# Kernel optimization log

Hardware: AMD Instinct MI355X
Metric: run time of the kernel (lower is better)

## Reference

```python
import jax, jax.numpy as jnp
import numpy as np

TP = 4
TOKENS = 8192
HIDDEN = 4096
EPS = 1e-6
FP8_MAX = 448.0  # float8_e4m3fn max


def setup_inputs() -> dict:
    key = jax.random.key(0)
    k1, k2, k3 = jax.random.split(key, 3)
    hidden_states = jax.random.normal(k1, (TP, TOKENS, HIDDEN), dtype=jnp.float32)
    residual = jax.random.normal(k2, (TOKENS, HIDDEN), dtype=jnp.float32)
    weight = jax.random.uniform(k3, (HIDDEN,), dtype=jnp.float32)
    return {"hidden_states": hidden_states, "residual": residual, "weight": weight}


def rms_norm(x, weight, eps):
    # vLLM RMSNorm: x * rsqrt(mean(x^2) + eps) * weight, computed in fp32
    var = jnp.mean(jnp.square(x), axis=-1, keepdims=True)
    return x * jax.lax.rsqrt(var + eps) * weight


def scaled_fp8_quant(x):
    # dynamic per-tensor fp8 quantization: scale = amax / FP8_MAX
    amax = jnp.max(jnp.abs(x))
    scale = jnp.maximum(amax, 1e-12) / FP8_MAX
    q = jnp.clip(x / scale, -FP8_MAX, FP8_MAX)  # quantized values (kept fp32 for reference math)
    return q, scale


def reference(hidden_states, residual, weight):
    # tensor_model_parallel_all_reduce == sum over TP shards (leading axis)
    all_reduce = jnp.sum(hidden_states, axis=0)  # [TOKENS, HIDDEN]
    normed = rms_norm(all_reduce, weight, EPS)
    q, scale = scaled_fp8_quant(normed)
    return q, scale
```

## Files before the change

kernel.cpp:

```cpp
#include <hip/hip_runtime.h>
#include <hip/hip_fp16.h>

#define TOKENS_ 8192
#define HIDDEN_ 4096
#define EPS_ 1e-6f
#define FP8MAX_ 448.0f

typedef float f32x4 __attribute__((ext_vector_type(4)));
typedef unsigned int u32x4 __attribute__((ext_vector_type(4)));

static constexpr size_t NELEM = (size_t)TOKENS_ * HIDDEN_;
static constexpr size_t WS_SCALE_OFF = 0;
static constexpr size_t WS_BMAX_OFF = 4096;
static constexpr size_t WS_H16_OFF = 65536;
static constexpr size_t WS_NEEDED = WS_H16_OFF + NELEM * sizeof(unsigned short);

static __device__ inline unsigned int pack_half2(float a, float b) {
    __half2 h = __floats2half2_rn(a, b);
    return *reinterpret_cast<unsigned int*>(&h);
}
static __device__ inline float2 unpack_half2(unsigned int u) {
    return __half22float2(*reinterpret_cast<const __half2*>(&u));
}
static __device__ inline float clip1(float x, float invs) {
    return fminf(fmaxf(x * invs, -FP8MAX_), FP8MAX_);
}

__global__ __launch_bounds__(256) void k_norm_h(
    const float* __restrict__ hs, const float* __restrict__ w,
    unsigned int* __restrict__ normed_h2, float* __restrict__ bmax_arr)
{
    const int row = blockIdx.x;
    const int tid = threadIdx.x;
    const size_t S4 = NELEM / 4;
    const f32x4* __restrict__ base =
        reinterpret_cast<const f32x4*>(hs) + (size_t)row * (HIDDEN_ / 4);
    const f32x4* __restrict__ w4 = reinterpret_cast<const f32x4*>(w);

    f32x4 sv[4];
    float ss = 0.f;
#pragma unroll
    for (int j = 0; j < 4; ++j) {
        const size_t idx = (size_t)tid + j * 256;
        f32x4 a = __builtin_nontemporal_load(&base[idx]);
        f32x4 b = __builtin_nontemporal_load(&base[idx + S4]);
        f32x4 c = __builtin_nontemporal_load(&base[idx + 2 * S4]);
        f32x4 d = __builtin_nontemporal_load(&base[idx + 3 * S4]);
        f32x4 s = (a + b) + (c + d);
        sv[j] = s;
        ss += s.x * s.x + s.y * s.y + s.z * s.z + s.w * s.w;
    }

    __shared__ float red[4];
#pragma unroll
    for (int off = 32; off > 0; off >>= 1) ss += __shfl_down(ss, off, 64);
    const int wave = tid >> 6;
    if ((tid & 63) == 0) red[wave] = ss;
    __syncthreads();
    ss = red[0] + red[1] + red[2] + red[3];
    const float inv = rsqrtf(ss * (1.0f / HIDDEN_) + EPS_);

    uint2* __restrict__ out =
        reinterpret_cast<uint2*>(normed_h2) + (size_t)row * (HIDDEN_ / 4);
    float am = 0.f;
#pragma unroll
    for (int j = 0; j < 4; ++j) {
        const size_t idx = (size_t)tid + j * 256;
        f32x4 wv = w4[idx];
        f32x4 o = sv[j] * inv * wv;
        uint2 p;
        p.x = pack_half2(o.x, o.y);
        p.y = pack_half2(o.z, o.w);
        out[idx] = p;
        am = fmaxf(am, fmaxf(fmaxf(fabsf(o.x), fabsf(o.y)),
                             fmaxf(fabsf(o.z), fabsf(o.w))));
    }

    __shared__ float redm[4];
#pragma unroll
    for (int off = 32; off > 0; off >>= 1)
        am = fmaxf(am, __shfl_down(am, off, 64));
    if ((tid & 63) == 0) redm[wave] = am;
    __syncthreads();
    if (tid == 0)
        bmax_arr[row] = fmaxf(fmaxf(redm[0], redm[1]), fmaxf(redm[2], redm[3]));
}

__global__ __launch_bounds__(256) void k_quant_h2(
    const unsigned int* __restrict__ normed_h2,
    const float* __restrict__ bmax_arr, float* __restrict__ q_out,
    float* __restrict__ scale_out)
{
    const int tid = threadIdx.x;
    const f32x4* __restrict__ b4 = reinterpret_cast<const f32x4*>(bmax_arr);
    float am = 0.f;
#pragma unroll
    for (int j = 0; j < 8; ++j) {
        f32x4 v = b4[tid + j * 256];
        am = fmaxf(am, fmaxf(fmaxf(v.x, v.y), fmaxf(v.z, v.w)));
    }
    __shared__ float red[4];
#pragma unroll
    for (int off = 32; off > 0; off >>= 1)
        am = fmaxf(am, __shfl_down(am, off, 64));
    if ((tid & 63) == 0) red[tid >> 6] = am;
    __syncthreads();
    am = fmaxf(fmaxf(red[0], red[1]), fmaxf(red[2], red[3]));
    const float scale = fmaxf(am, 1e-12f) / FP8MAX_;
    const float invs = 1.0f / scale;
    if (blockIdx.x == 0 && tid == 0) scale_out[0] = scale;

    const size_t n8 = NELEM / 8;
    const u32x4* __restrict__ src = reinterpret_cast<const u32x4*>(normed_h2);
    f32x4* __restrict__ dst = reinterpret_cast<f32x4*>(q_out);
    const size_t stride = (size_t)gridDim.x * blockDim.x;
    for (size_t i = (size_t)blockIdx.x * blockDim.x + tid; i < n8;
         i += stride) {
        u32x4 u = src[i];
        float2 f0 = unpack_half2(u.x);
        float2 f1 = unpack_half2(u.y);
        float2 f2 = unpack_half2(u.z);
        float2 f3 = unpack_half2(u.w);
        f32x4 a, b;
        a.x = clip1(f0.x, invs);
        a.y = clip1(f0.y, invs);
        a.z = clip1(f1.x, invs);
        a.w = clip1(f1.y, invs);
        b.x = clip1(f2.x, invs);
        b.y = clip1(f2.y, invs);
        b.z = clip1(f3.x, invs);
        b.w = clip1(f3.y, invs);
        __builtin_nontemporal_store(a, &dst[i * 2]);
        __builtin_nontemporal_store(b, &dst[i * 2 + 1]);
    }
}


__global__ __launch_bounds__(256) void k_fused_norm_f(
    const float* __restrict__ hs, const float* __restrict__ w,
    float* __restrict__ normed, float* __restrict__ bmax_arr)
{
    const int row = blockIdx.x;
    const int tid = threadIdx.x;
    const size_t S4 = NELEM / 4;
    const f32x4* __restrict__ base =
        reinterpret_cast<const f32x4*>(hs) + (size_t)row * (HIDDEN_ / 4);
    const f32x4* __restrict__ w4 = reinterpret_cast<const f32x4*>(w);
    f32x4 sv[4];
    float ss = 0.f;
#pragma unroll
    for (int j = 0; j < 4; ++j) {
        const size_t idx = (size_t)tid + j * 256;
        f32x4 a = base[idx];
        f32x4 b = base[idx + S4];
        f32x4 c = base[idx + 2 * S4];
        f32x4 d = base[idx + 3 * S4];
        f32x4 s = (a + b) + (c + d);
        sv[j] = s;
        ss += s.x * s.x + s.y * s.y + s.z * s.z + s.w * s.w;
    }
    __shared__ float red[4];
#pragma unroll
    for (int off = 32; off > 0; off >>= 1) ss += __shfl_down(ss, off, 64);
    const int wave = tid >> 6;
    if ((tid & 63) == 0) red[wave] = ss;
    __syncthreads();
    ss = red[0] + red[1] + red[2] + red[3];
    const float inv = rsqrtf(ss * (1.0f / HIDDEN_) + EPS_);
    f32x4* __restrict__ out =
        reinterpret_cast<f32x4*>(normed) + (size_t)row * (HIDDEN_ / 4);
    float am = 0.f;
#pragma unroll
    for (int j = 0; j < 4; ++j) {
        const size_t idx = (size_t)tid + j * 256;
        f32x4 wv = w4[idx];
        f32x4 o = sv[j] * inv * wv;
        out[idx] = o;
        am = fmaxf(am, fmaxf(fmaxf(fabsf(o.x), fabsf(o.y)),
                             fmaxf(fabsf(o.z), fabsf(o.w))));
    }
    __shared__ float redm[4];
#pragma unroll
    for (int off = 32; off > 0; off >>= 1)
        am = fmaxf(am, __shfl_down(am, off, 64));
    if ((tid & 63) == 0) redm[wave] = am;
    __syncthreads();
    if (tid == 0)
        bmax_arr[row] = fmaxf(fmaxf(redm[0], redm[1]), fmaxf(redm[2], redm[3]));
}

__global__ __launch_bounds__(256) void k_quant_f2(
    float* __restrict__ data, const float* __restrict__ bmax_arr,
    float* __restrict__ scale_out)
{
    const int tid = threadIdx.x;
    const f32x4* __restrict__ b4 = reinterpret_cast<const f32x4*>(bmax_arr);
    float am = 0.f;
#pragma unroll
    for (int j = 0; j < 8; ++j) {
        f32x4 v = b4[tid + j * 256];
        am = fmaxf(am, fmaxf(fmaxf(v.x, v.y), fmaxf(v.z, v.w)));
    }
    __shared__ float red[4];
#pragma unroll
    for (int off = 32; off > 0; off >>= 1)
        am = fmaxf(am, __shfl_down(am, off, 64));
    if ((tid & 63) == 0) red[tid >> 6] = am;
    __syncthreads();
    am = fmaxf(fmaxf(red[0], red[1]), fmaxf(red[2], red[3]));
    const float scale = fmaxf(am, 1e-12f) / FP8MAX_;
    const float invs = 1.0f / scale;
    if (blockIdx.x == 0 && tid == 0) scale_out[0] = scale;

    const size_t n4 = NELEM / 4;
    f32x4* __restrict__ d4 = reinterpret_cast<f32x4*>(data);
    const size_t stride = (size_t)gridDim.x * blockDim.x;
    for (size_t i = (size_t)blockIdx.x * blockDim.x + tid; i < n4;
         i += stride) {
        f32x4 v = d4[i];
        v.x = clip1(v.x, invs);
        v.y = clip1(v.y, invs);
        v.z = clip1(v.z, invs);
        v.w = clip1(v.w, invs);
        d4[i] = v;
    }
}

extern "C" void kernel_launch(void* const* d_in, const int* in_sizes, int n_in,
                              void* d_out, int out_size, void* d_ws, size_t ws_size,
                              hipStream_t stream) {
    const float* hs = (const float*)d_in[0];
    const float* w  = (const float*)d_in[2];
    float* out = (float*)d_out;
    float* scale_out = out + NELEM;
    float* bmax_arr = (float*)((char*)d_ws + WS_BMAX_OFF);

    if (ws_size >= WS_NEEDED) {
        unsigned int* normed_h2 = (unsigned int*)((char*)d_ws + WS_H16_OFF);
        k_norm_h<<<TOKENS_, 256, 0, stream>>>(hs, w, normed_h2, bmax_arr);
        k_quant_h2<<<2048, 256, 0, stream>>>(normed_h2, bmax_arr, out,
                                             scale_out);
    } else {
        k_fused_norm_f<<<TOKENS_, 256, 0, stream>>>(hs, w, out, bmax_arr);
        k_quant_f2<<<2048, 256, 0, stream>>>(out, bmax_arr, scale_out);
    }
}
```

Before: 150.1 us.

## Fuse norm and quantize into one cooperative kernel with grid sync

Replaces the two-launch norm-then-quantize pipeline with a single cooperative kernel of 1024 blocks, each handling 8 rows. A grid-wide sync sits between the per-row norm/amax phase and the quantize phase. Each block then re-reads the fp16 intermediate for its own rows, which may still be cache-resident. This removes one launch and the inter-kernel gap, but adds grid-sync cost and lower parallelism per phase. The fp32 fallback for small workspace is removed, so the fp16 workspace is now assumed to exist.

```diff
diff --git a/kernel.cpp b/kernel.cpp
--- a/kernel.cpp
+++ b/kernel.cpp
@@ -1,5 +1,8 @@
 #include <hip/hip_runtime.h>
 #include <hip/hip_fp16.h>
+#include <hip/hip_cooperative_groups.h>
+
+namespace cg = cooperative_groups;
 
 #define TOKENS_ 8192
 #define HIDDEN_ 4096
@@ -10,7 +13,6 @@
 typedef unsigned int u32x4 __attribute__((ext_vector_type(4)));
 
 static constexpr size_t NELEM = (size_t)TOKENS_ * HIDDEN_;
-static constexpr size_t WS_SCALE_OFF = 0;
 static constexpr size_t WS_BMAX_OFF = 4096;
 static constexpr size_t WS_H16_OFF = 65536;
 static constexpr size_t WS_NEEDED = WS_H16_OFF + NELEM * sizeof(unsigned short);
@@ -25,6 +27,115 @@
 static __device__ inline float clip1(float x, float invs) {
     return fminf(fmaxf(x * invs, -FP8MAX_), FP8MAX_);
 }
+
+__global__ __launch_bounds__(256) void k_coop2(
+    const float* __restrict__ hs, const float* __restrict__ w,
+    unsigned int* __restrict__ normed_h2, float* __restrict__ q_out,
+    float* __restrict__ scale_out, float* __restrict__ bmax_arr)
+{
+    const int tid = threadIdx.x;
+    const int wave = tid >> 6;
+    const int row0 = blockIdx.x * 8;
+    const size_t S4 = NELEM / 4;
+    const f32x4* __restrict__ w4 = reinterpret_cast<const f32x4*>(w);
+
+    __shared__ float red[4];
+    __shared__ float redm[4];
+
+    for (int r = 0; r < 8; ++r) {
+        const int row = row0 + r;
+        const f32x4* __restrict__ base =
+            reinterpret_cast<const f32x4*>(hs) + (size_t)row * (HIDDEN_ / 4);
+
+        f32x4 sv[4];
+        float ss = 0.f;
+#pragma unroll
+        for (int j = 0; j < 4; ++j) {
+            const size_t idx = (size_t)tid + j * 256;
+            f32x4 a = __builtin_nontemporal_load(&base[idx]);
+            f32x4 b = __builtin_nontemporal_load(&base[idx + S4]);
+            f32x4 c = __builtin_nontemporal_load(&base[idx + 2 * S4]);
+            f32x4 d = __builtin_nontemporal_load(&base[idx + 3 * S4]);
+            f32x4 s = (a + b) + (c + d);
+            sv[j] = s;
+            ss += s.x * s.x + s.y * s.y + s.z * s.z + s.w * s.w;
+        }
+#pragma unroll
+        for (int off = 32; off > 0; off >>= 1) ss += __shfl_down(ss, off, 64);
+        if ((tid & 63) == 0) red[wave] = ss;
+        __syncthreads();
+        ss = red[0] + red[1] + red[2] + red[3];
+        const float inv = rsqrtf(ss * (1.0f / HIDDEN_) + EPS_);
+
+        uint2* __restrict__ out =
+            reinterpret_cast<uint2*>(normed_h2) + (size_t)row * (HIDDEN_ / 4);
+        float am = 0.f;
+#pragma unroll
+        for (int j = 0; j < 4; ++j) {
+            const size_t idx = (size_t)tid + j * 256;
+            f32x4 wv = w4[idx];
+            f32x4 o = sv[j] * inv * wv;
+            uint2 p;
+            p.x = pack_half2(o.x, o.y);
+            p.y = pack_half2(o.z, o.w);
+            out[idx] = p;
+            am = fmaxf(am, fmaxf(fmaxf(fabsf(o.x), fabsf(o.y)),
+                                 fmaxf(fabsf(o.z), fabsf(o.w))));
+        }
+#pragma unroll
+        for (int off = 32; off > 0; off >>= 1)
+            am = fmaxf(am, __shfl_down(am, off, 64));
+        if ((tid & 63) == 0) redm[wave] = am;
+        __syncthreads();
+        if (tid == 0)
+            bmax_arr[row] =
+                fmaxf(fmaxf(redm[0], redm[1]), fmaxf(redm[2], redm[3]));
+    }
+    __threadfence();
+
+    cg::this_grid().sync();
+
+    const f32x4* __restrict__ b4 = reinterpret_cast<const f32x4*>(bmax_arr);
+    float am = 0.f;
+#pragma unroll
+    for (int j = 0; j < 8; ++j) {
+        f32x4 v = b4[tid + j * 256];
+        am = fmaxf(am, fmaxf(fmaxf(v.x, v.y), fmaxf(v.z, v.w)));
+    }
+#pragma unroll
+    for (int off = 32; off > 0; off >>= 1)
+        am = fmaxf(am, __shfl_down(am, off, 64));
+    __syncthreads();
+    if ((tid & 63) == 0) red[wave] = am;
+    __syncthreads();
+    am = fmaxf(fmaxf(red[0], red[1]), fmaxf(red[2], red[3]));
+    const float scale = fmaxf(am, 1e-12f) / FP8MAX_;
+    const float invs = 1.0f / scale;
+    if (blockIdx.x == 0 && tid == 0) scale_out[0] = scale;
+
+    for (int r = 0; r < 8; ++r) {
+        const int row = row0 + r;
+        const uint2* __restrict__ src =
+            reinterpret_cast<const uint2*>(normed_h2) +
+            (size_t)row * (HIDDEN_ / 4);
+        f32x4* __restrict__ dst =
+            reinterpret_cast<f32x4*>(q_out) + (size_t)row * (HIDDEN_ / 4);
+#pragma unroll
+        for (int j = 0; j < 4; ++j) {
+            const size_t idx = (size_t)tid + j * 256;
+            uint2 u = src[idx];
+            float2 f0 = unpack_half2(u.x);
+            float2 f1 = unpack_half2(u.y);
+            f32x4 o;
+            o.x = clip1(f0.x, invs);
+            o.y = clip1(f0.y, invs);
+            o.z = clip1(f1.x, invs);
+            o.w = clip1(f1.y, invs);
+            __builtin_nontemporal_store(o, &dst[idx]);
+        }
+    }
+}
+
 
 __global__ __launch_bounds__(256) void k_norm_h(
     const float* __restrict__ hs, const float* __restrict__ w,
@@ -50,7 +161,6 @@
         sv[j] = s;
         ss += s.x * s.x + s.y * s.y + s.z * s.z + s.w * s.w;
     }
-
     __shared__ float red[4];
 #pragma unroll
     for (int off = 32; off > 0; off >>= 1) ss += __shfl_down(ss, off, 64);
@@ -75,7 +185,6 @@
         am = fmaxf(am, fmaxf(fmaxf(fabsf(o.x), fabsf(o.y)),
                              fmaxf(fabsf(o.z), fabsf(o.w))));
     }
-
     __shared__ float redm[4];
 #pragma unroll
     for (int off = 32; off > 0; off >>= 1)
@@ -135,97 +244,6 @@
     }
 }
 
-
-__global__ __launch_bounds__(256) void k_fused_norm_f(
-    const float* __restrict__ hs, const float* __restrict__ w,
-    float* __restrict__ normed, float* __restrict__ bmax_arr)
-{
-    const int row = blockIdx.x;
-    const int tid = threadIdx.x;
-    const size_t S4 = NELEM / 4;
-    const f32x4* __restrict__ base =
-        reinterpret_cast<const f32x4*>(hs) + (size_t)row * (HIDDEN_ / 4);
-    const f32x4* __restrict__ w4 = reinterpret_cast<const f32x4*>(w);
-    f32x4 sv[4];
-    float ss = 0.f;
-#pragma unroll
-    for (int j = 0; j < 4; ++j) {
-        const size_t idx = (size_t)tid + j * 256;
-        f32x4 a = base[idx];
-        f32x4 b = base[idx + S4];
-        f32x4 c = base[idx + 2 * S4];
-        f32x4 d = base[idx + 3 * S4];
-        f32x4 s = (a + b) + (c + d);
-        sv[j] = s;
-        ss += s.x * s.x + s.y * s.y + s.z * s.z + s.w * s.w;
-    }
-    __shared__ float red[4];
-#pragma unroll
-    for (int off = 32; off > 0; off >>= 1) ss += __shfl_down(ss, off, 64);
-    const int wave = tid >> 6;
-    if ((tid & 63) == 0) red[wave] = ss;
-    __syncthreads();
-    ss = red[0] + red[1] + red[2] + red[3];
-    const float inv = rsqrtf(ss * (1.0f / HIDDEN_) + EPS_);
-    f32x4* __restrict__ out =
-        reinterpret_cast<f32x4*>(normed) + (size_t)row * (HIDDEN_ / 4);
-    float am = 0.f;
-#pragma unroll
-    for (int j = 0; j < 4; ++j) {
-        const size_t idx = (size_t)tid + j * 256;
-        f32x4 wv = w4[idx];
-        f32x4 o = sv[j] * inv * wv;
-        out[idx] = o;
-        am = fmaxf(am, fmaxf(fmaxf(fabsf(o.x), fabsf(o.y)),
-                             fmaxf(fabsf(o.z), fabsf(o.w))));
-    }
-    __shared__ float redm[4];
-#pragma unroll
-    for (int off = 32; off > 0; off >>= 1)
-        am = fmaxf(am, __shfl_down(am, off, 64));
-    if ((tid & 63) == 0) redm[wave] = am;
-    __syncthreads();
-    if (tid == 0)
-        bmax_arr[row] = fmaxf(fmaxf(redm[0], redm[1]), fmaxf(redm[2], redm[3]));
-}
-
-__global__ __launch_bounds__(256) void k_quant_f2(
-    float* __restrict__ data, const float* __restrict__ bmax_arr,
-    float* __restrict__ scale_out)
-{
-    const int tid = threadIdx.x;
-    const f32x4* __restrict__ b4 = reinterpret_cast<const f32x4*>(bmax_arr);
-    float am = 0.f;
-#pragma unroll
-    for (int j = 0; j < 8; ++j) {
-        f32x4 v = b4[tid + j * 256];
-        am = fmaxf(am, fmaxf(fmaxf(v.x, v.y), fmaxf(v.z, v.w)));
-    }
-    __shared__ float red[4];
-#pragma unroll
-    for (int off = 32; off > 0; off >>= 1)
-        am = fmaxf(am, __shfl_down(am, off, 64));
-    if ((tid & 63) == 0) red[tid >> 6] = am;
-    __syncthreads();
-    am = fmaxf(fmaxf(red[0], red[1]), fmaxf(red[2], red[3]));
-    const float scale = fmaxf(am, 1e-12f) / FP8MAX_;
-    const float invs = 1.0f / scale;
-    if (blockIdx.x == 0 && tid == 0) scale_out[0] = scale;
-
-    const size_t n4 = NELEM / 4;
-    f32x4* __restrict__ d4 = reinterpret_cast<f32x4*>(data);
-    const size_t stride = (size_t)gridDim.x * blockDim.x;
-    for (size_t i = (size_t)blockIdx.x * blockDim.x + tid; i < n4;
-         i += stride) {
-        f32x4 v = d4[i];
-        v.x = clip1(v.x, invs);
-        v.y = clip1(v.y, invs);
-        v.z = clip1(v.z, invs);
-        v.w = clip1(v.w, invs);
-        d4[i] = v;
-    }
-}
-
 extern "C" void kernel_launch(void* const* d_in, const int* in_sizes, int n_in,
                               void* d_out, int out_size, void* d_ws, size_t ws_size,
                               hipStream_t stream) {
@@ -234,14 +252,15 @@
     float* out = (float*)d_out;
     float* scale_out = out + NELEM;
     float* bmax_arr = (float*)((char*)d_ws + WS_BMAX_OFF);
-
-    if (ws_size >= WS_NEEDED) {
-        unsigned int* normed_h2 = (unsigned int*)((char*)d_ws + WS_H16_OFF);
+    unsigned int* normed_h2 = (unsigned int*)((char*)d_ws + WS_H16_OFF);
+
+    void* args[] = {(void*)&hs, (void*)&w, (void*)&normed_h2, (void*)&out,
+                    (void*)&scale_out, (void*)&bmax_arr};
+    hipError_t err = hipLaunchCooperativeKernel(
+        (const void*)k_coop2, dim3(1024), dim3(256), args, 0, stream);
+    if (err != hipSuccess) {
         k_norm_h<<<TOKENS_, 256, 0, stream>>>(hs, w, normed_h2, bmax_arr);
         k_quant_h2<<<2048, 256, 0, stream>>>(normed_h2, bmax_arr, out,
                                              scale_out);
-    } else {
-        k_fused_norm_f<<<TOKENS_, 256, 0, stream>>>(hs, w, out, bmax_arr);
-        k_quant_f2<<<2048, 256, 0, stream>>>(out, bmax_arr, scale_out);
-    }
-}
+    }
+}
```

Result: slower. 442.1 us (+194.6%).
